# Performance work log

Hardware: AMD Instinct MI355X
Metric: run time of the kernel (lower is better)

The kernel has to match this reference:

```python
import jax, jax.numpy as jnp
import numpy as np

N_POINTS = 12288
FEAT_DIM = 16


def setup_inputs() -> dict:
    key = jax.random.key(0)
    feats = jax.random.normal(key, (N_POINTS, FEAT_DIM), dtype=jnp.float32)
    return {"feats": feats, "topK": 1}


def reference(feats, topK):
    """LOGG3D_ATTN eval path for a single point cloud (batch=1).

    feats: [N, D] post-spvcnn point features.
    1) self_attention -> scalar weight per point
    2) weight features, top-k select k = N*topK points
    3) SOP: mean second-order (outer-product) pooling, flatten, L2-normalize.
    """
    N, D = feats.shape
    inv_sqrt_d = 1.0 / jnp.sqrt(jnp.asarray(D, feats.dtype))
    # self-attention over points: [N, N] scores (the ridge-regime hot spot)
    scores = jnp.matmul(feats, feats.T) * inv_sqrt_d          # [N, N]
    attn = jax.nn.softmax(scores, axis=-1)                    # [N, N]
    ctx = jnp.matmul(attn, feats)                             # [N, D]
    weights = jax.nn.sigmoid(jnp.sum(ctx * feats, axis=-1, keepdims=True))  # [N, 1]

    weighted_feat = feats * weights                           # [N, D]
    k = int(N * topK)
    _, top_idx = jax.lax.top_k(weights[:, 0], k)              # [k]
    x = weighted_feat[top_idx][None, :, :]                    # [1, k, D]

    # SOP: mean outer-product pooling (signed_sqrt=False, do_fc=False)
    so = jnp.einsum('bnd,bne->bde', x, x) / k                 # [1, D, D]
    out = so.reshape(1, -1)                                   # [1, D*D]
    out = out / jnp.linalg.norm(out, axis=-1, keepdims=True)
    return out
```

## Files before the change

### kernel.cpp

```cpp
#include <hip/hip_runtime.h>
#include <hip/hip_bf16.h>
#include <math.h>


#define NP 12288
#define DD 16
#define JSPLIT 8
#define JCHUNK (NP / JSPLIT)
#define JT 512
#define NTILES (JCHUNK / JT)

typedef __attribute__((ext_vector_type(4))) float f32x4;
typedef __attribute__((ext_vector_type(8))) short s16x8;
typedef __attribute__((ext_vector_type(4))) short s16x4;

#if defined(__has_builtin)
#if __has_builtin(__builtin_amdgcn_mfma_f32_16x16x16bf16_1k)
#define HAVE_MFMA16_BUILTIN 1
#endif
#endif

static __device__ __forceinline__ f32x4 mfma16(s16x4 a, s16x4 b, f32x4 c) {
#ifdef HAVE_MFMA16_BUILTIN
    return __builtin_amdgcn_mfma_f32_16x16x16bf16_1k(a, b, c, 0, 0, 0);
#else
    f32x4 d;
    asm volatile("s_nop 1\n\t"
                 "v_mfma_f32_16x16x16_bf16 %0, %1, %2, %0"
                 : "=v"(d)
                 : "v"(a), "v"(b), "0"(c));
    return d;
#endif
}

static __device__ __forceinline__ short f2bf(float x) {
    __hip_bfloat16 h = __float2bfloat16(x);
    return __builtin_bit_cast(short, h);
}
static __device__ __forceinline__ float bf2f(short s) {
    unsigned u = ((unsigned)(unsigned short)s) << 16;
    return __builtin_bit_cast(float, u);
}

__global__ __launch_bounds__(256)
void prep(const float* __restrict__ feats,
          unsigned short* __restrict__ ghi, unsigned short* __restrict__ glo,
          unsigned short* __restrict__ shi, unsigned short* __restrict__ gFt)
{
    int q = blockIdx.x * 256 + threadIdx.x;
    int row = q >> 2, c0 = (q & 3) * 4;
    f32x4 v = *(const f32x4*)(feats + q * 4);
    s16x4 hv, lv, sv;
    #pragma unroll
    for (int k = 0; k < 4; ++k) {
        short hi = f2bf(v[k]);
        hv[k] = hi;
        lv[k] = f2bf(v[k] - bf2f(hi));
        sv[k] = f2bf(v[k] * 0.25f);
        gFt[(c0 + k) * NP + row] = (unsigned short)hi;
    }
    *(s16x4*)(ghi + q * 4) = hv;
    *(s16x4*)(glo + q * 4) = lv;
    *(s16x4*)(shi + q * 4) = sv;
}

__global__ __launch_bounds__(256)
void attn_mfma(const unsigned short* __restrict__ ghi,
               const unsigned short* __restrict__ glo,
               const unsigned short* __restrict__ shi,
               const unsigned short* __restrict__ gFt,
               float* __restrict__ ctx_part,
               float* __restrict__ l_part)
{
    __shared__ unsigned short hiT[JT * 16];
    __shared__ unsigned short loT[JT * 16];
    __shared__ unsigned short FtT[16 * JT];

    const int tid = threadIdx.x;
    const int wave = tid >> 6, lane = tid & 63;
    const int il = lane & 15, g = lane >> 4, h = g & 1, g4 = g * 4;
    const int bid = blockIdx.x;
    const int js = bid & 7;
    const int rowblk = bid >> 3;
    const int ibase = rowblk * 128 + wave * 32;
    const int jbase = js * JCHUNK;

    const s16x8 b32A = *(const s16x8*)(shi + (ibase + il) * 16 + h * 8);
    const s16x8 b32B = *(const s16x8*)(shi + (ibase + 16 + il) * 16 + h * 8);

    s16x4 ones; ones[0] = ones[1] = ones[2] = ones[3] = (short)0x3F80;
    const f32x4 kZero = {0.f, 0.f, 0.f, 0.f};
    f32x4 ctxA = kZero, ctxB = kZero, lA = kZero, lB = kZero;

    const char* aBase = (const char*)(g < 2 ? hiT : loT)
                        + ((il * 32 + h * 16) ^ ((il & 7) << 4));
    const char* vBase = (const char*)FtT + il * 1024;
    const int mv = (il & 7) << 3;

    for (int ti = 0; ti < NTILES; ++ti) {
        const int jb = jbase + ti * JT;
        {
            const char* gH = (const char*)(ghi + jb * 16);
            const char* gL = (const char*)(glo + jb * 16);
            const char* gF = (const char*)(gFt + jb);
            #pragma unroll
            for (int k = 0; k < 4; ++k) {
                int c = tid + (k << 8);
                int mR = ((c >> 1) & 7) << 4;
                int mF = ((c >> 6) & 7) << 4;
                s16x8 vh = *(const s16x8*)(gH + c * 16);
                s16x8 vl = *(const s16x8*)(gL + c * 16);
                s16x8 vf = *(const s16x8*)(gF + (c >> 6) * (NP * 2) + (c & 63) * 16);
                *(s16x8*)((char*)hiT + ((c * 16) ^ mR)) = vh;
                *(s16x8*)((char*)loT + ((c * 16) ^ mR)) = vl;
                *(s16x8*)((char*)FtT + ((c * 16) ^ mF)) = vf;
            }
        }
        __syncthreads();

        #pragma unroll 4
        for (int jg = 0; jg < JT / 16; ++jg) {
            const s16x8 a32 = *(const s16x8*)(aBase + jg * 512);
            const int vo = ((jg << 4) + g4) ^ mv;
            const s16x4 aVt = *(const s16x4*)(vBase + (vo << 1));
            f32x4 sa = __builtin_amdgcn_mfma_f32_16x16x32_bf16(a32, b32A, kZero, 0, 0, 0);
            f32x4 sb = __builtin_amdgcn_mfma_f32_16x16x32_bf16(a32, b32B, kZero, 0, 0, 0);
            s16x4 pA, pB;
            pA[0] = f2bf(__expf(sa[0]));  pA[1] = f2bf(__expf(sa[1]));
            pA[2] = f2bf(__expf(sa[2]));  pA[3] = f2bf(__expf(sa[3]));
            pB[0] = f2bf(__expf(sb[0]));  pB[1] = f2bf(__expf(sb[1]));
            pB[2] = f2bf(__expf(sb[2]));  pB[3] = f2bf(__expf(sb[3]));
            ctxA = mfma16(aVt, pA, ctxA);
            lA   = mfma16(ones, pA, lA);
            ctxB = mfma16(aVt, pB, ctxB);
            lB   = mfma16(ones, pB, lB);
        }
        __syncthreads();
    }

    asm volatile("s_nop 7\n\ts_nop 7" ::: );

    const int iA = ibase + il, iB = iA + 16;
    *(f32x4*)(ctx_part + (js * NP + iA) * 16 + g4) = ctxA;
    *(f32x4*)(ctx_part + (js * NP + iB) * 16 + g4) = ctxB;
    if (g == 0) {
        l_part[js * NP + iA] = lA[0];
        l_part[js * NP + iB] = lB[0];
    }
}

__global__ __launch_bounds__(256)
void weights_sop(const float* __restrict__ feats,
                 const float* __restrict__ ctx_part,
                 const float* __restrict__ l_part,
                 float* __restrict__ mpart)
{
    __shared__ float gw[64 * 16];
    const int tid = threadIdx.x;
    const int rb = blockIdx.x * 64;

    if (tid < 64) {
        const int row = rb + tid;
        f32x4 c0 = {0,0,0,0}, c1 = {0,0,0,0}, c2 = {0,0,0,0}, c3 = {0,0,0,0};
        float l = 0.f;
        #pragma unroll
        for (int js = 0; js < JSPLIT; ++js) {
            const float* p = ctx_part + (js * NP + row) * 16;
            c0 += *(const f32x4*)(p + 0);
            c1 += *(const f32x4*)(p + 4);
            c2 += *(const f32x4*)(p + 8);
            c3 += *(const f32x4*)(p + 12);
            l += l_part[js * NP + row];
        }
        const f32x4 f0 = *(const f32x4*)(feats + row * 16 + 0);
        const f32x4 f1 = *(const f32x4*)(feats + row * 16 + 4);
        const f32x4 f2 = *(const f32x4*)(feats + row * 16 + 8);
        const f32x4 f3 = *(const f32x4*)(feats + row * 16 + 12);
        float z = 0.f;
        #pragma unroll
        for (int k = 0; k < 4; ++k)
            z += c0[k]*f0[k] + c1[k]*f1[k] + c2[k]*f2[k] + c3[k]*f3[k];
        z /= l;
        const float w = 1.f / (1.f + __expf(-z));
        #pragma unroll
        for (int k = 0; k < 4; ++k) {
            gw[tid * 16 + 0 + k]  = w * f0[k];
            gw[tid * 16 + 4 + k]  = w * f1[k];
            gw[tid * 16 + 8 + k]  = w * f2[k];
            gw[tid * 16 + 12 + k] = w * f3[k];
        }
    }
    __syncthreads();

    const int d = tid >> 4, e = tid & 15;
    float acc = 0.f;
    #pragma unroll 4
    for (int r = 0; r < 64; ++r)
        acc += gw[r * 16 + d] * gw[r * 16 + e];
    mpart[blockIdx.x * 256 + tid] = acc;
}

__global__ __launch_bounds__(256)
void finalize(const float* __restrict__ mpart, float* __restrict__ out)
{
    __shared__ float red[4];
    const int tid = threadIdx.x;
    float m = 0.f;
    #pragma unroll 4
    for (int b = 0; b < 192; ++b) m += mpart[b * 256 + tid];

    float ss = m * m;
    #pragma unroll
    for (int msk = 32; msk >= 1; msk >>= 1) ss += __shfl_xor(ss, msk, 64);
    if ((tid & 63) == 0) red[tid >> 6] = ss;
    __syncthreads();
    const float tot = red[0] + red[1] + red[2] + red[3];
    out[tid] = m / sqrtf(tot);
}

extern "C" void kernel_launch(void* const* d_in, const int* in_sizes, int n_in,
                              void* d_out, int out_size, void* d_ws, size_t ws_size,
                              hipStream_t stream) {
    (void)n_in; (void)out_size; (void)ws_size;
    const float* feats = (const float*)d_in[0];

    char* w = (char*)d_ws;
    unsigned short* ghi = (unsigned short*)(w);
    unsigned short* glo = (unsigned short*)(w + 393216);
    unsigned short* shi = (unsigned short*)(w + 786432);
    unsigned short* gFt = (unsigned short*)(w + 1179648);
    float* ctxp = (float*)(w + 1572864);
    float* lp   = (float*)(w + 7864320);
    float* mp   = (float*)(w + 8257536);

    prep       <<<192, 256, 0, stream>>>(feats, ghi, glo, shi, gFt);
    attn_mfma  <<<768, 256, 0, stream>>>(ghi, glo, shi, gFt, ctxp, lp);
    weights_sop<<<192, 256, 0, stream>>>(feats, ctxp, lp, mp);
    finalize   <<<1,   256, 0, stream>>>(mp, (float*)d_out);
}
```

Measured before the change: 108.9 us.

## Drop hi/lo bf16 split for single bf16 QK, use exp2, widen J-split

The QK^T score computation no longer uses a split hi+lo bf16 representation with a 16x16x32 MFMA. It now uses a single bf16 16x16x16 MFMA, with log2(e)/sqrt(d) folded into the query scale so that exp2 replaces exp. The J dimension is split 16 ways instead of 8, with 384-wide tiles, doubling the grid. The prep kernel transposes through LDS for coalesced writes, and weights_sop uses all threads for the partial reduction. Together these cut MFMA work, LDS traffic and exp cost, at the price of lower score precision and larger partial buffers to reduce.

```diff
diff --git a/kernel.cpp b/kernel.cpp
--- a/kernel.cpp
+++ b/kernel.cpp
@@ -4,11 +4,13 @@
 
 
 #define NP 12288
-#define DD 16
-#define JSPLIT 8
+#define JSPLIT 16
 #define JCHUNK (NP / JSPLIT)
-#define JT 512
+#define JT 384
 #define NTILES (JCHUNK / JT)
+#define JGPT (JT / 16)
+
+#define QSCALE 0.3606737602222839f
 
 typedef __attribute__((ext_vector_type(4))) float f32x4;
 typedef __attribute__((ext_vector_type(8))) short s16x8;
@@ -18,6 +20,12 @@
 #if __has_builtin(__builtin_amdgcn_mfma_f32_16x16x16bf16_1k)
 #define HAVE_MFMA16_BUILTIN 1
 #endif
+#if __has_builtin(__builtin_amdgcn_exp2f)
+#define EXP2F(x) __builtin_amdgcn_exp2f(x)
+#endif
+#endif
+#ifndef EXP2F
+#define EXP2F(x) exp2f(x)
 #endif
 
 static __device__ __forceinline__ f32x4 mfma16(s16x4 a, s16x4 b, f32x4 c) {
@@ -37,102 +45,103 @@
     __hip_bfloat16 h = __float2bfloat16(x);
     return __builtin_bit_cast(short, h);
 }
-static __device__ __forceinline__ float bf2f(short s) {
-    unsigned u = ((unsigned)(unsigned short)s) << 16;
-    return __builtin_bit_cast(float, u);
-}
 
 __global__ __launch_bounds__(256)
 void prep(const float* __restrict__ feats,
-          unsigned short* __restrict__ ghi, unsigned short* __restrict__ glo,
-          unsigned short* __restrict__ shi, unsigned short* __restrict__ gFt)
-{
-    int q = blockIdx.x * 256 + threadIdx.x;
-    int row = q >> 2, c0 = (q & 3) * 4;
-    f32x4 v = *(const f32x4*)(feats + q * 4);
-    s16x4 hv, lv, sv;
+          unsigned short* __restrict__ ghi, unsigned short* __restrict__ shi,
+          unsigned short* __restrict__ gFt)
+{
+    __shared__ unsigned short tr[64 * 16];
+    const int tid = threadIdx.x;
+    const int rowbase = blockIdx.x * 64;
+
+    const f32x4 v = *(const f32x4*)(feats + (size_t)rowbase * 16 + tid * 4);
+    s16x4 hv, sv;
     #pragma unroll
     for (int k = 0; k < 4; ++k) {
-        short hi = f2bf(v[k]);
-        hv[k] = hi;
-        lv[k] = f2bf(v[k] - bf2f(hi));
-        sv[k] = f2bf(v[k] * 0.25f);
-        gFt[(c0 + k) * NP + row] = (unsigned short)hi;
-    }
-    *(s16x4*)(ghi + q * 4) = hv;
-    *(s16x4*)(glo + q * 4) = lv;
-    *(s16x4*)(shi + q * 4) = sv;
+        hv[k] = f2bf(v[k]);
+        sv[k] = f2bf(v[k] * QSCALE);
+    }
+    *(s16x4*)(ghi + (size_t)rowbase * 16 + tid * 4) = hv;
+    *(s16x4*)(shi + (size_t)rowbase * 16 + tid * 4) = sv;
+    *(s16x4*)(tr + (tid >> 2) * 16 + (tid & 3) * 4) = hv;
+    __syncthreads();
+
+    if (tid < 128) {
+        const int p = tid >> 3, q8 = tid & 7;
+        s16x8 o;
+        #pragma unroll
+        for (int e = 0; e < 8; ++e) o[e] = (short)tr[(q8 * 8 + e) * 16 + p];
+        *(s16x8*)(gFt + (size_t)p * NP + rowbase + q8 * 8) = o;
+    }
 }
 
 __global__ __launch_bounds__(256)
 void attn_mfma(const unsigned short* __restrict__ ghi,
-               const unsigned short* __restrict__ glo,
                const unsigned short* __restrict__ shi,
                const unsigned short* __restrict__ gFt,
                float* __restrict__ ctx_part,
                float* __restrict__ l_part)
 {
     __shared__ unsigned short hiT[JT * 16];
-    __shared__ unsigned short loT[JT * 16];
     __shared__ unsigned short FtT[16 * JT];
 
     const int tid = threadIdx.x;
     const int wave = tid >> 6, lane = tid & 63;
-    const int il = lane & 15, g = lane >> 4, h = g & 1, g4 = g * 4;
-    const int bid = blockIdx.x;
-    const int js = bid & 7;
-    const int rowblk = bid >> 3;
+    const int il = lane & 15, g = lane >> 4, g4 = g * 4, g8 = g * 8;
+    const int js = blockIdx.x & (JSPLIT - 1);
+    const int rowblk = blockIdx.x >> 4;
     const int ibase = rowblk * 128 + wave * 32;
     const int jbase = js * JCHUNK;
 
-    const s16x8 b32A = *(const s16x8*)(shi + (ibase + il) * 16 + h * 8);
-    const s16x8 b32B = *(const s16x8*)(shi + (ibase + 16 + il) * 16 + h * 8);
+    const s16x4 bA = *(const s16x4*)(shi + (size_t)(ibase + il) * 16 + g4);
+    const s16x4 bB = *(const s16x4*)(shi + (size_t)(ibase + 16 + il) * 16 + g4);
 
     s16x4 ones; ones[0] = ones[1] = ones[2] = ones[3] = (short)0x3F80;
     const f32x4 kZero = {0.f, 0.f, 0.f, 0.f};
     f32x4 ctxA = kZero, ctxB = kZero, lA = kZero, lB = kZero;
 
-    const char* aBase = (const char*)(g < 2 ? hiT : loT)
-                        + ((il * 32 + h * 16) ^ ((il & 7) << 4));
-    const char* vBase = (const char*)FtT + il * 1024;
-    const int mv = (il & 7) << 3;
+    const char* aBase = (const char*)hiT + ((il * 32 + g8) ^ ((il & 7) << 4));
+    const char* vPlane = (const char*)FtT + il * (JT * 2);
+    const int vKey = (il & 7) << 4;
+
+    const int fp = tid >> 4, fq = tid & 15;
 
     for (int ti = 0; ti < NTILES; ++ti) {
         const int jb = jbase + ti * JT;
         {
-            const char* gH = (const char*)(ghi + jb * 16);
-            const char* gL = (const char*)(glo + jb * 16);
-            const char* gF = (const char*)(gFt + jb);
+            const char* gH = (const char*)ghi + (size_t)jb * 32;
             #pragma unroll
-            for (int k = 0; k < 4; ++k) {
-                int c = tid + (k << 8);
-                int mR = ((c >> 1) & 7) << 4;
-                int mF = ((c >> 6) & 7) << 4;
-                s16x8 vh = *(const s16x8*)(gH + c * 16);
-                s16x8 vl = *(const s16x8*)(gL + c * 16);
-                s16x8 vf = *(const s16x8*)(gF + (c >> 6) * (NP * 2) + (c & 63) * 16);
-                *(s16x8*)((char*)hiT + ((c * 16) ^ mR)) = vh;
-                *(s16x8*)((char*)loT + ((c * 16) ^ mR)) = vl;
-                *(s16x8*)((char*)FtT + ((c * 16) ^ mF)) = vf;
+            for (int k = 0; k < 3; ++k) {
+                const int c = tid + (k << 8);
+                s16x8 v = *(const s16x8*)(gH + c * 16);
+                *(s16x8*)((char*)hiT + ((c * 16) ^ (((c >> 1) & 7) << 4))) = v;
+            }
+            const char* gF = (const char*)gFt + (size_t)fp * (NP * 2) + (size_t)jb * 2;
+            #pragma unroll
+            for (int k = 0; k < 3; ++k) {
+                const int cq = fq + (k << 4);
+                s16x8 v = *(const s16x8*)(gF + cq * 16);
+                *(s16x8*)((char*)FtT + fp * (JT * 2)
+                          + ((cq * 16) ^ ((fp & 7) << 4))) = v;
             }
         }
         __syncthreads();
 
         #pragma unroll 4
-        for (int jg = 0; jg < JT / 16; ++jg) {
-            const s16x8 a32 = *(const s16x8*)(aBase + jg * 512);
-            const int vo = ((jg << 4) + g4) ^ mv;
-            const s16x4 aVt = *(const s16x4*)(vBase + (vo << 1));
-            f32x4 sa = __builtin_amdgcn_mfma_f32_16x16x32_bf16(a32, b32A, kZero, 0, 0, 0);
-            f32x4 sb = __builtin_amdgcn_mfma_f32_16x16x32_bf16(a32, b32B, kZero, 0, 0, 0);
+        for (int jg = 0; jg < JGPT; ++jg) {
+            const s16x4 aS = *(const s16x4*)(aBase + jg * 512);
+            const s16x4 aV = *(const s16x4*)(vPlane + (((jg << 5) + g8) ^ vKey));
+            const f32x4 sa = mfma16(aS, bA, kZero);
+            const f32x4 sb = mfma16(aS, bB, kZero);
             s16x4 pA, pB;
-            pA[0] = f2bf(__expf(sa[0]));  pA[1] = f2bf(__expf(sa[1]));
-            pA[2] = f2bf(__expf(sa[2]));  pA[3] = f2bf(__expf(sa[3]));
-            pB[0] = f2bf(__expf(sb[0]));  pB[1] = f2bf(__expf(sb[1]));
-            pB[2] = f2bf(__expf(sb[2]));  pB[3] = f2bf(__expf(sb[3]));
-            ctxA = mfma16(aVt, pA, ctxA);
+            pA[0] = f2bf(EXP2F(sa[0]));  pA[1] = f2bf(EXP2F(sa[1]));
+            pA[2] = f2bf(EXP2F(sa[2]));  pA[3] = f2bf(EXP2F(sa[3]));
+            pB[0] = f2bf(EXP2F(sb[0]));  pB[1] = f2bf(EXP2F(sb[1]));
+            pB[2] = f2bf(EXP2F(sb[2]));  pB[3] = f2bf(EXP2F(sb[3]));
+            ctxA = mfma16(aV, pA, ctxA);
             lA   = mfma16(ones, pA, lA);
-            ctxB = mfma16(aVt, pB, ctxB);
+            ctxB = mfma16(aV, pB, ctxB);
             lB   = mfma16(ones, pB, lB);
         }
         __syncthreads();
@@ -141,63 +150,49 @@
     asm volatile("s_nop 7\n\ts_nop 7" ::: );
 
     const int iA = ibase + il, iB = iA + 16;
-    *(f32x4*)(ctx_part + (js * NP + iA) * 16 + g4) = ctxA;
-    *(f32x4*)(ctx_part + (js * NP + iB) * 16 + g4) = ctxB;
+    *(f32x4*)(ctx_part + ((size_t)js * NP + iA) * 16 + g4) = ctxA;
+    *(f32x4*)(ctx_part + ((size_t)js * NP + iB) * 16 + g4) = ctxB;
     if (g == 0) {
-        l_part[js * NP + iA] = lA[0];
-        l_part[js * NP + iB] = lB[0];
+        l_part[(size_t)js * NP + iA] = lA[0];
+        l_part[(size_t)js * NP + iB] = lB[0];
     }
 }
 
 __global__ __launch_bounds__(256)
 void weights_sop(const float* __restrict__ feats,
-                 const float* __restrict__ ctx_part,
-                 const float* __restrict__ l_part,
+                 const float* __restrict__ ctxp,
+                 const float* __restrict__ lp,
                  float* __restrict__ mpart)
 {
     __shared__ float gw[64 * 16];
     const int tid = threadIdx.x;
-    const int rb = blockIdx.x * 64;
-
-    if (tid < 64) {
-        const int row = rb + tid;
-        f32x4 c0 = {0,0,0,0}, c1 = {0,0,0,0}, c2 = {0,0,0,0}, c3 = {0,0,0,0};
-        float l = 0.f;
-        #pragma unroll
-        for (int js = 0; js < JSPLIT; ++js) {
-            const float* p = ctx_part + (js * NP + row) * 16;
-            c0 += *(const f32x4*)(p + 0);
-            c1 += *(const f32x4*)(p + 4);
-            c2 += *(const f32x4*)(p + 8);
-            c3 += *(const f32x4*)(p + 12);
-            l += l_part[js * NP + row];
-        }
-        const f32x4 f0 = *(const f32x4*)(feats + row * 16 + 0);
-        const f32x4 f1 = *(const f32x4*)(feats + row * 16 + 4);
-        const f32x4 f2 = *(const f32x4*)(feats + row * 16 + 8);
-        const f32x4 f3 = *(const f32x4*)(feats + row * 16 + 12);
-        float z = 0.f;
-        #pragma unroll
-        for (int k = 0; k < 4; ++k)
-            z += c0[k]*f0[k] + c1[k]*f1[k] + c2[k]*f2[k] + c3[k]*f3[k];
-        z /= l;
-        const float w = 1.f / (1.f + __expf(-z));
-        #pragma unroll
-        for (int k = 0; k < 4; ++k) {
-            gw[tid * 16 + 0 + k]  = w * f0[k];
-            gw[tid * 16 + 4 + k]  = w * f1[k];
-            gw[tid * 16 + 8 + k]  = w * f2[k];
-            gw[tid * 16 + 12 + k] = w * f3[k];
-        }
-    }
+    const int rl = tid >> 2, q = tid & 3, d0 = q * 4;
+    const int row = blockIdx.x * 64 + rl;
+
+    f32x4 c = {0.f, 0.f, 0.f, 0.f};
+    float l = 0.f;
+    #pragma unroll
+    for (int js = 0; js < JSPLIT; ++js) {
+        c += *(const f32x4*)(ctxp + ((size_t)js * NP + row) * 16 + d0);
+        l += lp[(size_t)js * NP + row];
+    }
+    const f32x4 fv = *(const f32x4*)(feats + (size_t)row * 16 + d0);
+    float zp = c[0]*fv[0] + c[1]*fv[1] + c[2]*fv[2] + c[3]*fv[3];
+    zp += __shfl_xor(zp, 1, 64);
+    zp += __shfl_xor(zp, 2, 64);
+    const float z = zp / l;
+    const float w = 1.f / (1.f + EXP2F(-z * 1.4426950408889634f));
+
+    f32x4 gv; gv[0] = w*fv[0]; gv[1] = w*fv[1]; gv[2] = w*fv[2]; gv[3] = w*fv[3];
+    *(f32x4*)(gw + rl * 16 + d0) = gv;
     __syncthreads();
 
     const int d = tid >> 4, e = tid & 15;
     float acc = 0.f;
-    #pragma unroll 4
+    #pragma unroll 8
     for (int r = 0; r < 64; ++r)
         acc += gw[r * 16 + d] * gw[r * 16 + e];
-    mpart[blockIdx.x * 256 + tid] = acc;
+    mpart[(size_t)blockIdx.x * 256 + tid] = acc;
 }
 
 __global__ __launch_bounds__(256)
@@ -207,7 +202,7 @@
     const int tid = threadIdx.x;
     float m = 0.f;
     #pragma unroll 4
-    for (int b = 0; b < 192; ++b) m += mpart[b * 256 + tid];
+    for (int b = 0; b < 192; ++b) m += mpart[(size_t)b * 256 + tid];
 
     float ss = m * m;
     #pragma unroll
@@ -226,15 +221,14 @@
 
     char* w = (char*)d_ws;
     unsigned short* ghi = (unsigned short*)(w);
-    unsigned short* glo = (unsigned short*)(w + 393216);
-    unsigned short* shi = (unsigned short*)(w + 786432);
-    unsigned short* gFt = (unsigned short*)(w + 1179648);
-    float* ctxp = (float*)(w + 1572864);
-    float* lp   = (float*)(w + 7864320);
-    float* mp   = (float*)(w + 8257536);
-
-    prep       <<<192, 256, 0, stream>>>(feats, ghi, glo, shi, gFt);
-    attn_mfma  <<<768, 256, 0, stream>>>(ghi, glo, shi, gFt, ctxp, lp);
-    weights_sop<<<192, 256, 0, stream>>>(feats, ctxp, lp, mp);
-    finalize   <<<1,   256, 0, stream>>>(mp, (float*)d_out);
-}
+    unsigned short* shi = (unsigned short*)(w + 393216);
+    unsigned short* gFt = (unsigned short*)(w + 786432);
+    float* ctxp = (float*)(w + 1179648);
+    float* lp   = (float*)(w + 13762560);
+    float* mp   = (float*)(w + 14548992);
+
+    prep       <<<192,  256, 0, stream>>>(feats, ghi, shi, gFt);
+    attn_mfma  <<<1536, 256, 0, stream>>>(ghi, shi, gFt, ctxp, lp);
+    weights_sop<<<192,  256, 0, stream>>>(feats, ctxp, lp, mp);
+    finalize   <<<1,    256, 0, stream>>>(mp, (float*)d_out);
+}
```

After: 106.2 us. 2.5% less time.
